# Kernel optimization log

Measured on AMD Instinct MI355X. Metric: run time of the kernel, lower is better.

The kernel has to match this reference:

```python
import jax, jax.numpy as jnp
import numpy as np


def setup_inputs() -> dict:
    key = jax.random.key(0)
    k1, k2, k3, k4 = jax.random.split(key, 4)
    B, D, H, W, N = 32, 16, 256, 256, 512
    pred_batch = jax.random.normal(k1, (B, D, H, W), dtype=jnp.float32)
    kpt_batch = jax.random.uniform(k2, (B, N, 2), dtype=jnp.float32)  # normalized coords in [0,1)
    vis_batch = jax.random.randint(k3, (B, N), 0, 2, dtype=jnp.int32)
    tag_batch = jax.random.randint(k4, (B, N), 0, 32, dtype=jnp.int32)
    return {"pred_batch": pred_batch, "kpt_batch": kpt_batch,
            "vis_batch": vis_batch, "tag_batch": tag_batch}


def reference(pred_batch, kpt_batch, vis_batch, tag_batch):
    B, D, H, W = pred_batch.shape
    dt = pred_batch.dtype
    # unnorm with [W, H] then floor to integer pixel indices (as in original)
    unnorm = jnp.array([W, H], dtype=dt)
    idx = jnp.floor(kpt_batch * unnorm).astype(jnp.int32)   # [B, N, 2]
    y, x = idx[..., 0], idx[..., 1]
    # gather embeddings at keypoint locations: [B, D, N]
    pred_ebd = jax.vmap(lambda p, yy, xx: p[:, yy, xx])(pred_batch, y, x)
    # visibility mask replaces the variable-length boolean selection
    mask = (vis_batch > 0).astype(dt)                       # [B, N]
    pair_mask = mask[:, :, None] * mask[:, None, :]         # [B, N, N]
    true_sim = (tag_batch[:, :, None] == tag_batch[:, None, :]).astype(dt)
    # exponent = mean_d (a_d - b_d)^2 = mean(a^2) + mean(b^2) - 2/D * a.b
    sq = jnp.mean(pred_ebd ** 2, axis=1)                    # [B, N]
    dot = jnp.einsum('bdn,bdm->bnm', pred_ebd, pred_ebd) / D
    exponent = sq[:, :, None] + sq[:, None, :] - 2.0 * dot  # [B, N, N]
    pred_sim = 2.0 / (1.0 + jnp.exp(exponent))
    wgt = jnp.where((true_sim > 0) | (pred_sim > 0), jnp.asarray(10.0, dt), jnp.asarray(0.0, dt))
    dis = (pred_sim - true_sim) ** 2
    K = jnp.sum(mask, axis=1)                               # visible count per sample
    denom = jnp.maximum(K * K, 1.0)
    per_sample = jnp.sum(dis * wgt * pair_mask, axis=(1, 2)) / denom
    return jnp.mean(per_sample)
```

## Files before the change

### kernel.cpp

```cpp
#include <hip/hip_runtime.h>
#include <math.h>

#define B_ 32
#define D_ 16
#define H_ 256
#define W_ 256
#define N_ 512

__global__ __launch_bounds__(256) void gather_k(const float* __restrict__ pred,
                                                const float* __restrict__ kpt,
                                                float* __restrict__ ebd) {
    int bi = blockIdx.x;
    int b = bi >> 3;
    int part = bi & 7;
    int t = threadIdx.x;
#pragma unroll
    for (int j = 0; j < 4; ++j) {
        int e = part * 1024 + t + j * 256;
        int n = e >> 4;
        int d = e & 15;
        float k0 = kpt[(b * N_ + n) * 2 + 0];
        float k1 = kpt[(b * N_ + n) * 2 + 1];
        int y = (int)floorf(k0 * (float)W_);
        int x = (int)floorf(k1 * (float)H_);
        y = min(max(y, 0), H_ - 1);
        x = min(max(x, 0), W_ - 1);
        ebd[(size_t)b * (N_ * D_) + e] =
            pred[(((size_t)b * D_ + d) * H_ + y) * W_ + x];
    }
}

__global__ __launch_bounds__(256) void pair_k(const float* __restrict__ ebd,
                                              const int* __restrict__ vis,
                                              const int* __restrict__ tag,
                                              float* __restrict__ out) {
    __shared__ float4 es[N_ * 4];
    __shared__ int tg[N_];
    __shared__ float ms[N_];
    __shared__ float racc[4], rk[4];

    int bi = blockIdx.x;
    int b = bi >> 3;
    int nt = bi & 7;
    int t = threadIdx.x;

    const float4* eg = (const float4*)(ebd + (size_t)b * (N_ * D_));
#pragma unroll
    for (int i = t; i < N_ * 4; i += 256) es[i] = eg[i];
    for (int i = t; i < N_; i += 256) {
        tg[i] = tag[b * N_ + i];
        ms[i] = (vis[b * N_ + i] > 0) ? 1.0f : 0.0f;
    }
    __syncthreads();

    float kpart = ms[t] + ms[t + 256];

    int n = nt * 64 + (t >> 2);
    int q = t & 3;
    float4 a0 = es[n * 4 + 0], a1 = es[n * 4 + 1];
    float4 a2 = es[n * 4 + 2], a3 = es[n * 4 + 3];
    int tn = tg[n];
    float mn = ms[n];

    float acc = 0.0f;
    for (int i = 0; i < 128; ++i) {
        int m = i * 4 + q;
        float4 b0 = es[m * 4 + 0], b1 = es[m * 4 + 1];
        float4 b2 = es[m * 4 + 2], b3 = es[m * 4 + 3];
        float s, dd;
        dd = a0.x - b0.x; s  = dd * dd;
        dd = a0.y - b0.y; s += dd * dd;
        dd = a0.z - b0.z; s += dd * dd;
        dd = a0.w - b0.w; s += dd * dd;
        dd = a1.x - b1.x; s += dd * dd;
        dd = a1.y - b1.y; s += dd * dd;
        dd = a1.z - b1.z; s += dd * dd;
        dd = a1.w - b1.w; s += dd * dd;
        dd = a2.x - b2.x; s += dd * dd;
        dd = a2.y - b2.y; s += dd * dd;
        dd = a2.z - b2.z; s += dd * dd;
        dd = a2.w - b2.w; s += dd * dd;
        dd = a3.x - b3.x; s += dd * dd;
        dd = a3.y - b3.y; s += dd * dd;
        dd = a3.z - b3.z; s += dd * dd;
        dd = a3.w - b3.w; s += dd * dd;
        float ex = s * (1.0f / 16.0f);
        float ps = 2.0f / (1.0f + __expf(ex));
        float ts = (tn == tg[m]) ? 1.0f : 0.0f;
        float w  = (ts > 0.0f || ps > 0.0f) ? 10.0f : 0.0f;
        float di = ps - ts;
        acc += di * di * w * (mn * ms[m]);
    }

#pragma unroll
    for (int off = 32; off; off >>= 1) {
        acc   += __shfl_down(acc, off);
        kpart += __shfl_down(kpart, off);
    }
    if ((t & 63) == 0) { racc[t >> 6] = acc; rk[t >> 6] = kpart; }
    __syncthreads();
    if (t == 0) {
        float tot = racc[0] + racc[1] + racc[2] + racc[3];
        float K   = rk[0] + rk[1] + rk[2] + rk[3];
        float scale = 1.0f / (fmaxf(K * K, 1.0f) * (float)B_);
        atomicAdd(out, tot * scale);
    }
}

extern "C" void kernel_launch(void* const* d_in, const int* in_sizes, int n_in,
                              void* d_out, int out_size, void* d_ws, size_t ws_size,
                              hipStream_t stream) {
    const float* pred = (const float*)d_in[0];
    const float* kpt  = (const float*)d_in[1];
    const int*   vis  = (const int*)d_in[2];
    const int*   tag  = (const int*)d_in[3];
    float* out = (float*)d_out;
    float* ebd = (float*)d_ws;

    hipMemsetAsync(out, 0, sizeof(float), stream);
    gather_k<<<256, 256, 0, stream>>>(pred, kpt, ebd);
    pair_k<<<256, 256, 0, stream>>>(ebd, vis, tag, out);
}
```

Measured before the change: 204.7 us.

## Fuse gather into symmetric tiled pair kernel using norm-expansion dot product

Merges the gather and pairwise kernels into one launch. Each block handles one upper-triangular pair of 64-keypoint tiles and gathers both tiles straight from pred into shared memory, so the workspace round trip is gone. Symmetry halves the pairwise work: off-diagonal tiles are weighted by two. The squared distance is rewritten as norm terms minus a dot product, and the always-true weight test becomes a constant factor of ten. In exchange, each keypoint is gathered several times across blocks (once per tile pair it belongs to), and 1152 blocks now each issue an atomic add.

```diff
diff --git a/kernel.cpp b/kernel.cpp
--- a/kernel.cpp
+++ b/kernel.cpp
@@ -6,103 +6,107 @@
 #define H_ 256
 #define W_ 256
 #define N_ 512
+#define TS 64
+#define NT 8
+#define NPAIR 36
+#define RS 20
 
-__global__ __launch_bounds__(256) void gather_k(const float* __restrict__ pred,
-                                                const float* __restrict__ kpt,
-                                                float* __restrict__ ebd) {
+__global__ __launch_bounds__(256) void tagloss_k(const float* __restrict__ pred,
+                                                 const float* __restrict__ kpt,
+                                                 const int* __restrict__ vis,
+                                                 const int* __restrict__ tag,
+                                                 float* __restrict__ out) {
+    __shared__ float eA[TS * RS];
+    __shared__ float eB[TS * RS];
+    __shared__ float sqA[TS], sqB[TS];
+    __shared__ int   tgA[TS], tgB[TS];
+    __shared__ float msA[TS], msB[TS];
+    __shared__ float redA[4], redK[4];
+
     int bi = blockIdx.x;
-    int b = bi >> 3;
-    int part = bi & 7;
+    int b  = bi / NPAIR;
+    int p  = bi - b * NPAIR;
+    int ti = 0, rem = p;
+    while (rem >= (NT - ti)) { rem -= (NT - ti); ++ti; }
+    int tj = ti + rem;
+
     int t = threadIdx.x;
-#pragma unroll
-    for (int j = 0; j < 4; ++j) {
-        int e = part * 1024 + t + j * 256;
-        int n = e >> 4;
-        int d = e & 15;
+
+    {
+        int r    = t >> 1;
+        int half = t & 1;
+        int inA  = (r < TS);
+        int rr   = inA ? r : (r - TS);
+        int n    = (inA ? ti : tj) * TS + rr;
         float k0 = kpt[(b * N_ + n) * 2 + 0];
         float k1 = kpt[(b * N_ + n) * 2 + 1];
         int y = (int)floorf(k0 * (float)W_);
         int x = (int)floorf(k1 * (float)H_);
         y = min(max(y, 0), H_ - 1);
         x = min(max(x, 0), W_ - 1);
-        ebd[(size_t)b * (N_ * D_) + e] =
-            pred[(((size_t)b * D_ + d) * H_ + y) * W_ + x];
+        const float* pb = pred + (((size_t)b * D_ + half * 8) * H_ + y) * W_ + x;
+        float v[8];
+#pragma unroll
+        for (int dd = 0; dd < 8; ++dd) v[dd] = pb[(size_t)dd * (H_ * W_)];
+        float psum = 0.f;
+#pragma unroll
+        for (int dd = 0; dd < 8; ++dd) psum += v[dd] * v[dd];
+        float other = __shfl_xor(psum, 1);
+        float sqm = (psum + other) * (1.0f / (float)D_);
+
+        float* dst = (inA ? eA : eB) + rr * RS + half * 8;
+        ((float4*)dst)[0] = make_float4(v[0], v[1], v[2], v[3]);
+        ((float4*)dst)[1] = make_float4(v[4], v[5], v[6], v[7]);
+        if (half == 0) {
+            int   tgv = tag[b * N_ + n];
+            float msv = (vis[b * N_ + n] > 0) ? 1.0f : 0.0f;
+            if (inA) { sqA[rr] = sqm; tgA[rr] = tgv; msA[rr] = msv; }
+            else     { sqB[rr] = sqm; tgB[rr] = tgv; msB[rr] = msv; }
+        }
     }
-}
-
-__global__ __launch_bounds__(256) void pair_k(const float* __restrict__ ebd,
-                                              const int* __restrict__ vis,
-                                              const int* __restrict__ tag,
-                                              float* __restrict__ out) {
-    __shared__ float4 es[N_ * 4];
-    __shared__ int tg[N_];
-    __shared__ float ms[N_];
-    __shared__ float racc[4], rk[4];
-
-    int bi = blockIdx.x;
-    int b = bi >> 3;
-    int nt = bi & 7;
-    int t = threadIdx.x;
-
-    const float4* eg = (const float4*)(ebd + (size_t)b * (N_ * D_));
-#pragma unroll
-    for (int i = t; i < N_ * 4; i += 256) es[i] = eg[i];
-    for (int i = t; i < N_; i += 256) {
-        tg[i] = tag[b * N_ + i];
-        ms[i] = (vis[b * N_ + i] > 0) ? 1.0f : 0.0f;
-    }
+    float kpart = ((vis[b * N_ + t] > 0) ? 1.0f : 0.0f) +
+                  ((vis[b * N_ + t + 256] > 0) ? 1.0f : 0.0f);
     __syncthreads();
 
-    float kpart = ms[t] + ms[t + 256];
-
-    int n = nt * 64 + (t >> 2);
-    int q = t & 3;
-    float4 a0 = es[n * 4 + 0], a1 = es[n * 4 + 1];
-    float4 a2 = es[n * 4 + 2], a3 = es[n * 4 + 3];
-    int tn = tg[n];
-    float mn = ms[n];
+    int r2 = t >> 2;
+    int q  = t & 3;
+    const float4* ap = (const float4*)&eA[r2 * RS];
+    float4 a0 = ap[0], a1 = ap[1], a2 = ap[2], a3 = ap[3];
+    float sa = sqA[r2];
+    int   tn = tgA[r2];
+    float mn = msA[r2];
 
     float acc = 0.0f;
-    for (int i = 0; i < 128; ++i) {
-        int m = i * 4 + q;
-        float4 b0 = es[m * 4 + 0], b1 = es[m * 4 + 1];
-        float4 b2 = es[m * 4 + 2], b3 = es[m * 4 + 3];
-        float s, dd;
-        dd = a0.x - b0.x; s  = dd * dd;
-        dd = a0.y - b0.y; s += dd * dd;
-        dd = a0.z - b0.z; s += dd * dd;
-        dd = a0.w - b0.w; s += dd * dd;
-        dd = a1.x - b1.x; s += dd * dd;
-        dd = a1.y - b1.y; s += dd * dd;
-        dd = a1.z - b1.z; s += dd * dd;
-        dd = a1.w - b1.w; s += dd * dd;
-        dd = a2.x - b2.x; s += dd * dd;
-        dd = a2.y - b2.y; s += dd * dd;
-        dd = a2.z - b2.z; s += dd * dd;
-        dd = a2.w - b2.w; s += dd * dd;
-        dd = a3.x - b3.x; s += dd * dd;
-        dd = a3.y - b3.y; s += dd * dd;
-        dd = a3.z - b3.z; s += dd * dd;
-        dd = a3.w - b3.w; s += dd * dd;
-        float ex = s * (1.0f / 16.0f);
+#pragma unroll 4
+    for (int i = 0; i < 16; ++i) {
+        int m = (i << 2) | q;
+        const float4* bp = (const float4*)&eB[m * RS];
+        float4 b0 = bp[0], b1 = bp[1], b2 = bp[2], b3 = bp[3];
+        float dot;
+        dot  = a0.x * b0.x; dot += a0.y * b0.y; dot += a0.z * b0.z; dot += a0.w * b0.w;
+        dot += a1.x * b1.x; dot += a1.y * b1.y; dot += a1.z * b1.z; dot += a1.w * b1.w;
+        dot += a2.x * b2.x; dot += a2.y * b2.y; dot += a2.z * b2.z; dot += a2.w * b2.w;
+        dot += a3.x * b3.x; dot += a3.y * b3.y; dot += a3.z * b3.z; dot += a3.w * b3.w;
+        float ex = sa + sqB[m] - 0.125f * dot;
         float ps = 2.0f / (1.0f + __expf(ex));
-        float ts = (tn == tg[m]) ? 1.0f : 0.0f;
-        float w  = (ts > 0.0f || ps > 0.0f) ? 10.0f : 0.0f;
+        float ts = (tn == tgB[m]) ? 1.0f : 0.0f;
         float di = ps - ts;
-        acc += di * di * w * (mn * ms[m]);
+        acc += di * di * msB[m];
     }
+    acc *= mn;
 
 #pragma unroll
     for (int off = 32; off; off >>= 1) {
         acc   += __shfl_down(acc, off);
         kpart += __shfl_down(kpart, off);
     }
-    if ((t & 63) == 0) { racc[t >> 6] = acc; rk[t >> 6] = kpart; }
+    if ((t & 63) == 0) { redA[t >> 6] = acc; redK[t >> 6] = kpart; }
     __syncthreads();
     if (t == 0) {
-        float tot = racc[0] + racc[1] + racc[2] + racc[3];
-        float K   = rk[0] + rk[1] + rk[2] + rk[3];
-        float scale = 1.0f / (fmaxf(K * K, 1.0f) * (float)B_);
+        float tot = redA[0] + redA[1] + redA[2] + redA[3];
+        float K   = redK[0] + redK[1] + redK[2] + redK[3];
+        float tilew = (ti == tj) ? 1.0f : 2.0f;
+        float scale = 10.0f * tilew / (fmaxf(K * K, 1.0f) * (float)B_);
         atomicAdd(out, tot * scale);
     }
 }
@@ -115,9 +119,7 @@
     const int*   vis  = (const int*)d_in[2];
     const int*   tag  = (const int*)d_in[3];
     float* out = (float*)d_out;
-    float* ebd = (float*)d_ws;
 
-    hipMemsetAsync(out, 0, sizeof(float), stream);
-    gather_k<<<256, 256, 0, stream>>>(pred, kpt, ebd);
-    pair_k<<<256, 256, 0, stream>>>(ebd, vis, tag, out);
+    hipMemsetAsync(out, 0, sizeof(float) * out_size, stream);
+    tagloss_k<<<B_ * NPAIR, 256, 0, stream>>>(pred, kpt, vis, tag, out);
 }
```

Result: no change. 201.9 us (-1.4%).
